# Optimization experiments

Hardware: AMD Instinct MI355X
Metric: run time of the kernel (lower is better)

## Reference

```python
import jax, jax.numpy as jnp
import numpy as np

HIDDEN = 2048
HEADS = 16
HEAD_DIM = HIDDEN // HEADS
BATCH = 2
SEQ = 2048


def setup_inputs() -> dict:
    key = jax.random.key(0)
    ks = jax.random.split(key, 9)
    s = 0.02
    return {
        "x": jax.random.normal(ks[0], (BATCH, SEQ, HIDDEN), dtype=jnp.float32),
        "wq": jax.random.normal(ks[1], (HIDDEN, HIDDEN), dtype=jnp.float32) * s,
        "bq": jax.random.normal(ks[2], (HIDDEN,), dtype=jnp.float32) * s,
        "wk": jax.random.normal(ks[3], (HIDDEN, HIDDEN), dtype=jnp.float32) * s,
        "bk": jax.random.normal(ks[4], (HIDDEN,), dtype=jnp.float32) * s,
        "wv": jax.random.normal(ks[5], (HIDDEN, HIDDEN), dtype=jnp.float32) * s,
        "bv": jax.random.normal(ks[6], (HIDDEN,), dtype=jnp.float32) * s,
        "wo": jax.random.normal(ks[7], (HIDDEN, HIDDEN), dtype=jnp.float32) * s,
        "bo": jax.random.normal(ks[8], (HIDDEN,), dtype=jnp.float32) * s,
    }


def reference(x, wq, bq, wk, bk, wv, bv, wo, bo):
    B, S, _ = x.shape
    scale = jnp.sqrt(jnp.float32(HEAD_DIM))
    # torch Linear: y = x @ W.T + b
    def proj(w, b):
        return (x @ w.T + b).reshape(B, S, HEADS, HEAD_DIM).transpose(0, 2, 1, 3)
    q = proj(wq, bq)  # [B,H,S,D]
    k = proj(wk, bk)
    v = proj(wv, bv)
    scores = jnp.einsum("bhqd,bhkd->bhqk", q, k) / scale  # [B,H,S,S]
    probs = jax.nn.softmax(scores, axis=-1)
    ctx = jnp.einsum("bhqk,bhkd->bhqd", probs, v)  # [B,H,S,D]
    ctx = ctx.transpose(0, 2, 1, 3).reshape(B, S, HIDDEN)
    return ctx @ wo.T + bo
```

## Files before the change

kernel.cpp:

```cpp
#include <hip/hip_runtime.h>

typedef unsigned short u16;
typedef unsigned int   u32;
typedef float  f32x4   __attribute__((ext_vector_type(4)));
typedef __bf16 bf16x8  __attribute__((ext_vector_type(8)));
typedef u16    u16x8   __attribute__((ext_vector_type(8)));
typedef u16    u16x4   __attribute__((ext_vector_type(4)));
typedef u32    u32x2   __attribute__((ext_vector_type(2)));
typedef u32    u32x4   __attribute__((ext_vector_type(4)));

#define HIDDEN 2048
#define SEQ    2048
#define NHEADS 16
#define HD     128
#define BATCH  2
#define QSTR   4096

typedef const __attribute__((address_space(3))) u16* lptr;

__device__ __forceinline__ u16 f2bf(float f) {
  u32 u = __builtin_bit_cast(u32, f);
  u += 0x7FFFu + ((u >> 16) & 1u);
  return (u16)(u >> 16);
}
__device__ __forceinline__ u32 pk2(float a, float b) {
  __bf16 x = (__bf16)a, y = (__bf16)b;
  return (u32)__builtin_bit_cast(u16, x) | ((u32)__builtin_bit_cast(u16, y) << 16);
}
__device__ __forceinline__ bf16x8 ld_frag(const u16* p) {
  return __builtin_bit_cast(bf16x8, *(const u32x4*)p);
}
__device__ __forceinline__ void gload_lds16(const u16* g, u16* l) {
  __builtin_amdgcn_global_load_lds((const __attribute__((address_space(1))) u32*)g,
                                   (__attribute__((address_space(3))) u32*)l, 16, 0, 0);
}

#define DSR(dst, base, lit) \
  asm volatile("ds_read_b128 %0, %1 offset:" lit : "=v"(dst) : "v"(base))

#define MFMA16(d, a, b) d = __builtin_amdgcn_mfma_f32_16x16x32_bf16(a, b, d, 0, 0, 0)

__global__ __launch_bounds__(256) void cvt_kernel(const float* __restrict__ src,
                                                  u16* __restrict__ dst, int n4) {
  int stride = gridDim.x * blockDim.x;
  for (int i = blockIdx.x * blockDim.x + threadIdx.x; i < n4; i += stride) {
    f32x4 v = ((const f32x4*)src)[i];
    u16x4 o;
    o[0] = f2bf(v[0]); o[1] = f2bf(v[1]); o[2] = f2bf(v[2]); o[3] = f2bf(v[3]);
    *(u16x4*)(dst + (size_t)i * 4) = o;
  }
}

__global__ __launch_bounds__(256) void cvt4_kernel(
    const float* __restrict__ s0, const float* __restrict__ s1,
    const float* __restrict__ s2, const float* __restrict__ s3,
    u16* __restrict__ o0, u16* __restrict__ o1,
    u16* __restrict__ o2, u16* __restrict__ o3, int n4) {
  const float* src = (blockIdx.y == 0) ? s0 : (blockIdx.y == 1) ? s1 : (blockIdx.y == 2) ? s2 : s3;
  u16* dst = (blockIdx.y == 0) ? o0 : (blockIdx.y == 1) ? o1 : (blockIdx.y == 2) ? o2 : o3;
  int stride = gridDim.x * blockDim.x;
  for (int i = blockIdx.x * blockDim.x + threadIdx.x; i < n4; i += stride) {
    f32x4 v = ((const f32x4*)src)[i];
    u16x4 o;
    o[0] = f2bf(v[0]); o[1] = f2bf(v[1]); o[2] = f2bf(v[2]); o[3] = f2bf(v[3]);
    *(u16x4*)(dst + (size_t)i * 4) = o;
  }
}

__global__ __launch_bounds__(512, 2) void gemm_qkv(
    const u16* __restrict__ A, const u16* __restrict__ Bt,
    const float* __restrict__ bq, const float* __restrict__ bk,
    const float* __restrict__ bv,
    u16* __restrict__ qk, u16* __restrict__ vtb, float qscale)
{
  __shared__ __attribute__((aligned(16))) u16 As[2][16384];
  __shared__ __attribute__((aligned(16))) u16 Bs[2][12288];

  const int tid  = threadIdx.x;
  const int lane = tid & 63;
  const int wave = tid >> 6;
  const int l15  = lane & 15;
  const int g    = lane >> 4;
  const int wm   = wave >> 2;
  const int wn   = wave & 3;

  const int id  = blockIdx.x;
  const int xcd = id & 7;
  const int c   = id >> 3;
  const int tileN = (xcd * 4 + (c >> 4)) * 192;
  const int tileM = (c & 15) << 8;

  const int srow = tid >> 3;
  const int gch8 = ((tid & 7) ^ (srow & 7)) * 8;
  const u16* agp = A  + (size_t)(tileM + srow) * HIDDEN + gch8;
  const u16* bgp = Bt + (size_t)(tileN + srow) * HIDDEN + gch8;
  u16* asp = (u16*)&As[0][0] + tid * 8;
  u16* bsp = (u16*)&Bs[0][0] + tid * 8;

  auto stage = [&](int buf, int ko) {
    u16* ad = asp + buf * 16384;
    u16* bd = bsp + buf * 12288;
#pragma unroll
    for (int r = 0; r < 4; ++r)
      gload_lds16(agp + (size_t)r * 64 * HIDDEN + ko, ad + r * 4096);
#pragma unroll
    for (int r = 0; r < 3; ++r)
      gload_lds16(bgp + (size_t)r * 64 * HIDDEN + ko, bd + r * 4096);
  };

  const int sw = l15 & 7;
  const int c0 = (g ^ sw) * 8;
  const int c1 = ((g ^ sw) ^ 4) * 8;
  lptr aT = (lptr)&As[0][0] + (size_t)(wm * 128 + l15) * 64;
  lptr bT = (lptr)&Bs[0][0] + (size_t)(wn * 48 + l15) * 64;

  f32x4 acc[8][3] = {};
  bf16x8 Xa[8], Xb[3], Ya[8], Yb[3];

#define ISSUE_SET(Sa, Sb, ab, bb)      \
  DSR(Sa[0], ab, "0");                 \
  DSR(Sa[1], ab, "2048");              \
  DSR(Sa[2], ab, "4096");              \
  DSR(Sa[3], ab, "6144");              \
  DSR(Sa[4], ab, "8192");              \
  DSR(Sa[5], ab, "10240");             \
  DSR(Sa[6], ab, "12288");             \
  DSR(Sa[7], ab, "14336");             \
  DSR(Sb[0], bb, "0");                 \
  DSR(Sb[1], bb, "2048");              \
  DSR(Sb[2], bb, "4096");

#define MFMA24(Sa, Sb)                                                                    \
  _Pragma("unroll")                                                                       \
  for (int mf = 0; mf < 8; ++mf) {                                                        \
    _Pragma("unroll")                                                                     \
    for (int nf = 0; nf < 3; ++nf)                                                        \
      acc[mf][nf] = __builtin_amdgcn_mfma_f32_16x16x32_bf16(Sa[mf], Sb[nf], acc[mf][nf], 0, 0, 0); \
  }

  stage(0, 0);
  stage(1, 64);
  asm volatile("s_waitcnt vmcnt(7)" ::: "memory");
  __builtin_amdgcn_s_barrier();
  __builtin_amdgcn_sched_barrier(0);
  {
    lptr ab = aT + c0;
    lptr bb = bT + c0;
    ISSUE_SET(Xa, Xb, ab, bb)
  }

#pragma unroll 2
  for (int t = 0; t < 32; ++t) {
    const int cur = t & 1;
    lptr aC = aT + cur * 16384;
    lptr bC = bT + cur * 12288;
    {
      lptr ab = aC + c1;
      lptr bb = bC + c1;
      ISSUE_SET(Ya, Yb, ab, bb)
    }
    asm volatile("s_waitcnt lgkmcnt(11)" ::: "memory");
    __builtin_amdgcn_sched_barrier(0);
    __builtin_amdgcn_s_setprio(1);
    MFMA24(Xa, Xb)
    __builtin_amdgcn_s_setprio(0);
    asm volatile("s_waitcnt lgkmcnt(0)" ::: "memory");
    __builtin_amdgcn_sched_barrier(0);
    __builtin_amdgcn_s_setprio(1);
    MFMA24(Ya, Yb)
    __builtin_amdgcn_s_setprio(0);
    __builtin_amdgcn_s_barrier();
    __builtin_amdgcn_sched_barrier(0);
    if (t < 30) {
      stage(cur, (t + 2) * 64);
      asm volatile("s_waitcnt vmcnt(7)" ::: "memory");
    } else {
      asm volatile("s_waitcnt vmcnt(0)" ::: "memory");
    }
    __builtin_amdgcn_s_barrier();
    __builtin_amdgcn_sched_barrier(0);
    if (t < 31) {
      lptr ab = aT + (cur ^ 1) * 16384 + c0;
      lptr bb = bT + (cur ^ 1) * 12288 + c0;
      ISSUE_SET(Xa, Xb, ab, bb)
    }
  }

#pragma unroll
  for (int mi = 0; mi < 8; ++mi) {
#pragma unroll
    for (int ni = 0; ni < 3; ++ni) {
      const int gcb = tileN + wn * 48 + ni * 16;
      const int seg = gcb >> 11;
      const int gc  = gcb + l15;
      const float bvv = ((seg == 0) ? bq : (seg == 1) ? bk : bv)[gc & 2047];
      if (seg < 2) {
        const float scl = (seg == 0) ? qscale : 1.f;
#pragma unroll
        for (int j = 0; j < 4; ++j) {
          const int gr = tileM + wm * 128 + mi * 16 + g * 4 + j;
          qk[(size_t)gr * QSTR + gc] = f2bf((acc[mi][ni][j] + bvv) * scl);
        }
      } else {
        const int dglob = gc - 4096;
        const int hh = dglob >> 7, dd = dglob & 127;
        const int srow0 = tileM + wm * 128 + mi * 16 + g * 4;
        const int bb = srow0 >> 11, ss = srow0 & 2047;
        u16x4 o;
#pragma unroll
        for (int j = 0; j < 4; ++j) o[j] = f2bf(acc[mi][ni][j] + bvv);
        *(u16x4*)(vtb + ((size_t)((bb * NHEADS + hh) * HD + dd)) * SEQ + ss) = o;
      }
    }
  }
#undef ISSUE_SET
#undef MFMA24
}

__global__ __launch_bounds__(256, 2) void gemm_bt(
    const u16* __restrict__ A, const u16* __restrict__ Bt,
    const float* __restrict__ bias, float* __restrict__ Cout,
    int M, int N, int K)
{
  __shared__ __attribute__((aligned(16))) u16 As[128 * 32];
  __shared__ __attribute__((aligned(16))) u16 Bs[128 * 32];
  const int tid  = threadIdx.x;
  const int lane = tid & 63;
  const int wave = tid >> 6;

  const int nbx   = N >> 7;
  const int nby   = M >> 7;
  const int id    = blockIdx.x;
  const int xcd   = id & 7;
  const int c     = id >> 3;
  const int cpx   = nbx >> 3;
  const int tileN = (xcd * cpx + c / nby) << 7;
  const int tileM = (c % nby) << 7;

  const int g = lane >> 4, r = lane & 15;

  const int srow = lane >> 2;
  const int scol = (lane & 3) * 8;
  const u16* ag0 = A  + (size_t)(tileM + wave * 16 + srow) * K + scol;
  const u16* ag1 = ag0 + (size_t)64 * K;
  const u16* bg0 = Bt + (size_t)(tileN + wave * 16 + srow) * K + scol;
  const u16* bg1 = bg0 + (size_t)64 * K;
  u16* as0 = &As[wave * 512];
  u16* as1 = &As[(wave + 4) * 512];
  u16* bs0 = &Bs[wave * 512];
  u16* bs1 = &Bs[(wave + 4) * 512];

  const int wm = wave >> 1, wn = wave & 1;
  const u16* afp = &As[(wm * 64 + r) * 32 + g * 8];
  const u16* bfp = &Bs[(wn * 64 + r) * 32 + g * 8];

  f32x4 acc[4][4] = {};

  for (int kt = 0; kt < K; kt += 32) {
    __syncthreads();
    gload_lds16(ag0 + kt, as0);
    gload_lds16(ag1 + kt, as1);
    gload_lds16(bg0 + kt, bs0);
    gload_lds16(bg1 + kt, bs1);
    __syncthreads();
    bf16x8 af[4], bf[4];
#pragma unroll
    for (int mi = 0; mi < 4; mi++) af[mi] = ld_frag(afp + mi * 512);
#pragma unroll
    for (int ni = 0; ni < 4; ni++) bf[ni] = ld_frag(bfp + ni * 512);
#pragma unroll
    for (int mi = 0; mi < 4; mi++)
#pragma unroll
      for (int ni = 0; ni < 4; ni++)
        acc[mi][ni] = __builtin_amdgcn_mfma_f32_16x16x32_bf16(af[mi], bf[ni], acc[mi][ni], 0, 0, 0);
  }

#pragma unroll
  for (int mi = 0; mi < 4; mi++) {
#pragma unroll
    for (int ni = 0; ni < 4; ni++) {
      const int gc = tileN + wn * 64 + ni * 16 + r;
      const float bv = bias[gc];
#pragma unroll
      for (int j = 0; j < 4; j++) {
        const int gr = tileM + wm * 64 + mi * 16 + g * 4 + j;
        Cout[(size_t)gr * N + gc] = acc[mi][ni][j] + bv;
      }
    }
  }
}

__global__ __launch_bounds__(256, 2) void attn_kernel(
    const u16* __restrict__ QKg, const u16* __restrict__ Vtg, u16* __restrict__ Ctx)
{
  __shared__ __attribute__((aligned(16))) u16 Ks[2][64 * 128];
  __shared__ __attribute__((aligned(16))) u16 Vs[2][128 * 64];

  const int tid  = threadIdx.x;
  const int lane = tid & 63;
  const int wave = tid >> 6;
  const int g4   = lane >> 4;
  const int l15  = lane & 15;

  const int wg = ((blockIdx.x & 7) << 6) + (blockIdx.x >> 3);
  const int bh = wg >> 4;
  const int qt = wg & 15;
  const int b  = bh >> 4, h = bh & 15;

  const u16* Qb  = QKg + (size_t)b * SEQ * QSTR + (size_t)h * HD;
  const u16* Kb  = Qb + 2048;
  const u16* Vth = Vtg + (size_t)bh * HD * SEQ;
  u16* Cb = Ctx + (size_t)b * SEQ * HIDDEN + (size_t)h * HD;

  const int qbase = qt * 128 + wave * 32 + l15;

  bf16x8 qf[2][4];
#pragma unroll
  for (int qs = 0; qs < 2; qs++)
#pragma unroll
    for (int dc = 0; dc < 4; dc++)
      qf[qs][dc] = ld_frag(Qb + (size_t)(qbase + qs * 16) * QSTR + dc * 32 + g4 * 8);

  const int kvp0 = (l15 >> 2) * 8 + (l15 & 3);
  const int msw  = (l15 & 3) | (((l15 >> 2) & 1) << 2);
  const int msw3 = msw & 3;
  const int mk   = (l15 >> 2) & 1;
  const int kcol = (g4 ^ msw3) * 8;

  lptr ksb = (lptr)&Ks[0][0];
  lptr kE0 = ksb + (kvp0      ) * 128 + kcol + mk * 32;
  lptr kO0 = ksb + (kvp0      ) * 128 + kcol + (1 ^ mk) * 32;
  lptr kE1 = ksb + (kvp0 +   4) * 128 + kcol + mk * 32;
  lptr kO1 = ksb + (kvp0 +   4) * 128 + kcol + (1 ^ mk) * 32;
  lptr kE2 = ksb + (kvp0 +  32) * 128 + kcol + mk * 32;
  lptr kO2 = ksb + (kvp0 +  32) * 128 + kcol + (1 ^ mk) * 32;
  lptr kE3 = ksb + (kvp0 +  36) * 128 + kcol + mk * 32;
  lptr kO3 = ksb + (kvp0 +  36) * 128 + kcol + (1 ^ mk) * 32;

  lptr vsb = (lptr)&Vs[0][0];
  lptr vB0 = vsb + l15 * 64 + ((0 * 4 + g4) ^ (l15 & 7)) * 8;
  lptr vB1 = vsb + l15 * 64 + ((1 * 4 + g4) ^ (l15 & 7)) * 8;

  const u16* kg[4];
  const u16* vg[4];
  u16* ksd = (u16*)&Ks[0][0] + tid * 8;
  u16* vsd = (u16*)&Vs[0][0] + tid * 8;
#pragma unroll
  for (int i = 0; i < 4; i++) {
    const int idx = tid + i * 256;
    const int kv = idx >> 4, up = idx & 15;
    const int um = up ^ ((kv & 3) | (((kv >> 3) & 1) << 2));
    kg[i] = Kb + (size_t)kv * QSTR + um * 8;
    const int d = idx >> 3, u = idx & 7;
    const int uv = u ^ (d & 7);
    vg[i] = Vth + (size_t)d * SEQ + uv * 8;
  }

  auto stage = [&](int buf, int kv0) {
    u16* kd = ksd + buf * 8192;
    u16* vd = vsd + buf * 8192;
#pragma unroll
    for (int i = 0; i < 4; i++) gload_lds16(kg[i] + (size_t)kv0 * QSTR, kd + i * 2048);
#pragma unroll
    for (int i = 0; i < 4; i++) gload_lds16(vg[i] + kv0, vd + i * 2048);
  };

  f32x4 ctx[2][8] = {};
  float m_run[2] = {-1e30f, -1e30f};
  float l_run[2] = {0.f, 0.f};

  stage(0, 0);

  const int NT = SEQ / 64;
  for (int t = 0; t < NT; t++) {
    const int buf = t & 1;

    if (t + 1 < NT) {
      stage(buf ^ 1, (t + 1) * 64);
      asm volatile("s_waitcnt vmcnt(8)" ::: "memory");
    } else {
      asm volatile("s_waitcnt vmcnt(0)" ::: "memory");
    }
    __builtin_amdgcn_s_barrier();
    __builtin_amdgcn_sched_barrier(0);

    bf16x8 kf[4][4];
    {
      const int bo = buf * 8192;
      lptr e0 = kE0 + bo, o0 = kO0 + bo, e1 = kE1 + bo, o1 = kO1 + bo;
      lptr e2 = kE2 + bo, o2 = kO2 + bo, e3 = kE3 + bo, o3 = kO3 + bo;
      DSR(kf[0][0], e0, "0"); DSR(kf[0][1], o0, "0"); DSR(kf[0][2], e0, "128"); DSR(kf[0][3], o0, "128");
      DSR(kf[1][0], e1, "0"); DSR(kf[1][1], o1, "0"); DSR(kf[1][2], e1, "128"); DSR(kf[1][3], o1, "128");
      DSR(kf[2][0], e2, "0"); DSR(kf[2][1], o2, "0"); DSR(kf[2][2], e2, "128"); DSR(kf[2][3], o2, "128");
      DSR(kf[3][0], e3, "0"); DSR(kf[3][1], o3, "0"); DSR(kf[3][2], e3, "128"); DSR(kf[3][3], o3, "128");
    }
    f32x4 s[2][4] = {};
    asm volatile("s_waitcnt lgkmcnt(8)" ::: "memory");
    __builtin_amdgcn_sched_barrier(0);
    __builtin_amdgcn_s_setprio(1);
#pragma unroll
    for (int ni = 0; ni < 2; ni++)
#pragma unroll
      for (int dc = 0; dc < 4; dc++) {
        MFMA16(s[0][ni], kf[ni][dc], qf[0][dc]);
        MFMA16(s[1][ni], kf[ni][dc], qf[1][dc]);
      }
    __builtin_amdgcn_sched_barrier(0);
    asm volatile("s_waitcnt lgkmcnt(0)" ::: "memory");
    __builtin_amdgcn_sched_barrier(0);
#pragma unroll
    for (int ni = 2; ni < 4; ni++)
#pragma unroll
      for (int dc = 0; dc < 4; dc++) {
        MFMA16(s[0][ni], kf[ni][dc], qf[0][dc]);
        MFMA16(s[1][ni], kf[ni][dc], qf[1][dc]);
      }
    __builtin_amdgcn_s_setprio(0);
    __builtin_amdgcn_sched_barrier(0);

    float pmax[2];
#pragma unroll
    for (int qs = 0; qs < 2; qs++) {
      float m0 = fmaxf(fmaxf(s[qs][0][0], s[qs][0][1]), fmaxf(s[qs][0][2], s[qs][0][3]));
      float m1 = fmaxf(fmaxf(s[qs][1][0], s[qs][1][1]), fmaxf(s[qs][1][2], s[qs][1][3]));
      float m2 = fmaxf(fmaxf(s[qs][2][0], s[qs][2][1]), fmaxf(s[qs][2][2], s[qs][2][3]));
      float m3 = fmaxf(fmaxf(s[qs][3][0], s[qs][3][1]), fmaxf(s[qs][3][2], s[qs][3][3]));
      pmax[qs] = fmaxf(fmaxf(m0, m1), fmaxf(m2, m3));
      pmax[qs] = fmaxf(pmax[qs], __shfl_xor(pmax[qs], 16));
      pmax[qs] = fmaxf(pmax[qs], __shfl_xor(pmax[qs], 32));
    }
    const bool ok0 = (pmax[0] <= m_run[0] + 8.f);
    const bool ok1 = (pmax[1] <= m_run[1] + 8.f);
    if (!__all(ok0 && ok1)) {
#pragma unroll
      for (int qs = 0; qs < 2; qs++) {
        const float mn = fmaxf(m_run[qs], pmax[qs]);
        const float corr = exp2f(m_run[qs] - mn);
        m_run[qs] = mn;
        l_run[qs] *= corr;
#pragma unroll
        for (int dt = 0; dt < 8; dt++)
#pragma unroll
          for (int j = 0; j < 4; j++) ctx[qs][dt][j] *= corr;
      }
    }
    bf16x8 pfrag[2][2];
#pragma unroll
    for (int qs = 0; qs < 2; qs++) {
      float ps = 0.f;
#pragma unroll
      for (int ni = 0; ni < 4; ni++)
#pragma unroll
        for (int j = 0; j < 4; j++) {
          const float p = exp2f(s[qs][ni][j] - m_run[qs]);
          s[qs][ni][j] = p;
          ps += p;
        }
      ps += __shfl_xor(ps, 16);
      ps += __shfl_xor(ps, 32);
      l_run[qs] += ps;
#pragma unroll
      for (int hh = 0; hh < 2; hh++) {
        u32x4 pw;
        pw[0] = pk2(s[qs][2 * hh][0], s[qs][2 * hh][1]);
        pw[1] = pk2(s[qs][2 * hh][2], s[qs][2 * hh][3]);
        pw[2] = pk2(s[qs][2 * hh + 1][0], s[qs][2 * hh + 1][1]);
        pw[3] = pk2(s[qs][2 * hh + 1][2], s[qs][2 * hh + 1][3]);
        pfrag[qs][hh] = __builtin_bit_cast(bf16x8, pw);
      }
    }
    __builtin_amdgcn_sched_barrier(0);

    bf16x8 vf[2][8];
    {
      lptr v0 = vB0 + buf * 8192;
      lptr v1 = vB1 + buf * 8192;
      DSR(vf[0][0], v0, "0");     DSR(vf[0][1], v0, "2048");
      DSR(vf[0][2], v0, "4096");  DSR(vf[0][3], v0, "6144");
      DSR(vf[0][4], v0, "8192");  DSR(vf[0][5], v0, "10240");
      DSR(vf[0][6], v0, "12288"); DSR(vf[0][7], v0, "14336");
      DSR(vf[1][0], v1, "0");     DSR(vf[1][1], v1, "2048");
      DSR(vf[1][2], v1, "4096");  DSR(vf[1][3], v1, "6144");
      DSR(vf[1][4], v1, "8192");  DSR(vf[1][5], v1, "10240");
      DSR(vf[1][6], v1, "12288"); DSR(vf[1][7], v1, "14336");
    }
    asm volatile("s_waitcnt lgkmcnt(8)" ::: "memory");
    __builtin_amdgcn_sched_barrier(0);
    __builtin_amdgcn_s_setprio(1);
#pragma unroll
    for (int dt = 0; dt < 8; dt++) {
      MFMA16(ctx[0][dt], vf[0][dt], pfrag[0][0]);
      MFMA16(ctx[1][dt], vf[0][dt], pfrag[1][0]);
    }
    __builtin_amdgcn_sched_barrier(0);
    asm volatile("s_waitcnt lgkmcnt(0)" ::: "memory");
    __builtin_amdgcn_sched_barrier(0);
#pragma unroll
    for (int dt = 0; dt < 8; dt++) {
      MFMA16(ctx[0][dt], vf[1][dt], pfrag[0][1]);
      MFMA16(ctx[1][dt], vf[1][dt], pfrag[1][1]);
    }
    __builtin_amdgcn_s_setprio(0);
    __builtin_amdgcn_sched_barrier(0);

    __builtin_amdgcn_s_barrier();
    __builtin_amdgcn_sched_barrier(0);
  }

#pragma unroll
  for (int qs = 0; qs < 2; qs++) {
    const float linv = 1.f / l_run[qs];
    u16* crow = Cb + (size_t)(qbase + qs * 16) * HIDDEN;
#pragma unroll
    for (int dt = 0; dt < 8; dt++) {
      u16x4 o;
#pragma unroll
      for (int j = 0; j < 4; j++) o[j] = f2bf(ctx[qs][dt][j] * linv);
      *(u16x4*)&crow[dt * 16 + g4 * 4] = o;
    }
  }
}

extern "C" void kernel_launch(void* const* d_in, const int* in_sizes, int n_in,
                              void* d_out, int out_size, void* d_ws, size_t ws_size,
                              hipStream_t stream) {
  (void)in_sizes; (void)n_in; (void)out_size; (void)ws_size;
  const float* x  = (const float*)d_in[0];
  const float* wq = (const float*)d_in[1];
  const float* bq = (const float*)d_in[2];
  const float* wk = (const float*)d_in[3];
  const float* bk = (const float*)d_in[4];
  const float* wv = (const float*)d_in[5];
  const float* bv = (const float*)d_in[6];
  const float* wo = (const float*)d_in[7];
  const float* bo = (const float*)d_in[8];

  const size_t NX = (size_t)BATCH * SEQ * HIDDEN;
  const size_t NW = (size_t)HIDDEN * HIDDEN;
  u16* xb   = (u16*)d_ws;
  u16* wqb  = xb  + NX;
  u16* wkb  = wqb + NW;
  u16* wvb  = wkb + NW;
  u16* wob  = wvb + NW;
  u16* qk   = wob + NW;
  u16* vtb  = qk  + 2 * NX;
  u16* ctxb = xb;

  cvt_kernel<<<2048, 256, 0, stream>>>(x, xb, (int)(NX / 4));
  cvt4_kernel<<<dim3(512, 4), 256, 0, stream>>>(wq, wk, wv, wo, wqb, wkb, wvb, wob, (int)(NW / 4));

  const float qscale = 0.12751744174240807f;
  gemm_qkv<<<512, 512, 0, stream>>>(xb, wqb, bq, bk, bv, qk, vtb, qscale);

  attn_kernel<<<512, 256, 0, stream>>>(qk, vtb, ctxb);

  gemm_bt<<<512, 256, 0, stream>>>(ctxb, wob, bo, (float*)d_out, BATCH * SEQ, HIDDEN, HIDDEN);
}
```

Measured before the change: 277.8 us.

## Retile QKV GEMM to 256x128 blocks with BK=32 and defer softmax row-sum reduction

The QKV projection GEMM moves from 256x192 tiles with a 64-wide K step to 256x128 tiles with a 32-wide K step. LDS use per block drops, the launch bound rises to 4 blocks per CU, and the grid grows to 768 blocks, with a new XOR swizzle and a simpler single-buffered fragment load per step. The aim is higher occupancy and better latency hiding, at the cost of lower arithmetic intensity per tile and twice as many barrier-synchronised iterations. Separately, the attention kernel no longer does the cross-lane shuffle reduction of the softmax row sum on every KV tile. It keeps per-lane partial sums and reduces them once at the end, which is valid because all lanes share the same running max.

```diff
diff --git a/kernel.cpp b/kernel.cpp
--- a/kernel.cpp
+++ b/kernel.cpp
@@ -67,130 +67,100 @@
   }
 }
 
-__global__ __launch_bounds__(512, 2) void gemm_qkv(
+__global__ __launch_bounds__(512, 4) void gemm_qkv(
     const u16* __restrict__ A, const u16* __restrict__ Bt,
     const float* __restrict__ bq, const float* __restrict__ bk,
     const float* __restrict__ bv,
     u16* __restrict__ qk, u16* __restrict__ vtb, float qscale)
 {
-  __shared__ __attribute__((aligned(16))) u16 As[2][16384];
-  __shared__ __attribute__((aligned(16))) u16 Bs[2][12288];
+  __shared__ __attribute__((aligned(16))) u16 As[2][8192];
+  __shared__ __attribute__((aligned(16))) u16 Bs[2][4096];
 
   const int tid  = threadIdx.x;
   const int lane = tid & 63;
   const int wave = tid >> 6;
   const int l15  = lane & 15;
   const int g    = lane >> 4;
-  const int wm   = wave >> 2;
-  const int wn   = wave & 3;
+  const int wm   = wave >> 1;
+  const int wn   = wave & 1;
 
   const int id  = blockIdx.x;
   const int xcd = id & 7;
   const int c   = id >> 3;
-  const int tileN = (xcd * 4 + (c >> 4)) * 192;
+  const int tileN = (xcd * 6 + (c >> 4)) << 7;
   const int tileM = (c & 15) << 8;
 
-  const int srow = tid >> 3;
-  const int gch8 = ((tid & 7) ^ (srow & 7)) * 8;
-  const u16* agp = A  + (size_t)(tileM + srow) * HIDDEN + gch8;
-  const u16* bgp = Bt + (size_t)(tileN + srow) * HIDDEN + gch8;
+  const int sr   = tid >> 2;
+  const int su   = tid & 3;
+  const int skey = (sr ^ (sr >> 2)) & 3;
+  const int sgc  = (su ^ skey) * 8;
+  const u16* agp = A  + (size_t)(tileM + sr) * HIDDEN + sgc;
+  const u16* bgp = Bt + (size_t)(tileN + sr) * HIDDEN + sgc;
   u16* asp = (u16*)&As[0][0] + tid * 8;
   u16* bsp = (u16*)&Bs[0][0] + tid * 8;
 
   auto stage = [&](int buf, int ko) {
-    u16* ad = asp + buf * 16384;
-    u16* bd = bsp + buf * 12288;
-#pragma unroll
-    for (int r = 0; r < 4; ++r)
-      gload_lds16(agp + (size_t)r * 64 * HIDDEN + ko, ad + r * 4096);
-#pragma unroll
-    for (int r = 0; r < 3; ++r)
-      gload_lds16(bgp + (size_t)r * 64 * HIDDEN + ko, bd + r * 4096);
+    u16* ad = asp + buf * 8192;
+    gload_lds16(agp + ko, ad);
+    gload_lds16(agp + (size_t)128 * HIDDEN + ko, ad + 4096);
+    gload_lds16(bgp + ko, bsp + buf * 4096);
   };
 
-  const int sw = l15 & 7;
-  const int c0 = (g ^ sw) * 8;
-  const int c1 = ((g ^ sw) ^ 4) * 8;
-  lptr aT = (lptr)&As[0][0] + (size_t)(wm * 128 + l15) * 64;
-  lptr bT = (lptr)&Bs[0][0] + (size_t)(wn * 48 + l15) * 64;
-
-  f32x4 acc[8][3] = {};
-  bf16x8 Xa[8], Xb[3], Ya[8], Yb[3];
-
-#define ISSUE_SET(Sa, Sb, ab, bb)      \
-  DSR(Sa[0], ab, "0");                 \
-  DSR(Sa[1], ab, "2048");              \
-  DSR(Sa[2], ab, "4096");              \
-  DSR(Sa[3], ab, "6144");              \
-  DSR(Sa[4], ab, "8192");              \
-  DSR(Sa[5], ab, "10240");             \
-  DSR(Sa[6], ab, "12288");             \
-  DSR(Sa[7], ab, "14336");             \
-  DSR(Sb[0], bb, "0");                 \
-  DSR(Sb[1], bb, "2048");              \
-  DSR(Sb[2], bb, "4096");
-
-#define MFMA24(Sa, Sb)                                                                    \
-  _Pragma("unroll")                                                                       \
-  for (int mf = 0; mf < 8; ++mf) {                                                        \
-    _Pragma("unroll")                                                                     \
-    for (int nf = 0; nf < 3; ++nf)                                                        \
-      acc[mf][nf] = __builtin_amdgcn_mfma_f32_16x16x32_bf16(Sa[mf], Sb[nf], acc[mf][nf], 0, 0, 0); \
-  }
+  const int fkey = (l15 ^ (l15 >> 2)) & 3;
+  const int kch  = (g ^ fkey) * 8;
+  lptr aT = (lptr)&As[0][0] + (size_t)(wm * 64 + l15) * 32 + kch;
+  lptr bT = (lptr)&Bs[0][0] + (size_t)(wn * 64 + l15) * 32 + kch;
+
+  f32x4 acc[4][4] = {};
+  bf16x8 af[4], bf[4];
+
+#define ISSUE8(ab, bb)                                                              \
+  DSR(af[0], ab, "0"); DSR(af[1], ab, "1024"); DSR(af[2], ab, "2048"); DSR(af[3], ab, "3072"); \
+  DSR(bf[0], bb, "0"); DSR(bf[1], bb, "1024"); DSR(bf[2], bb, "2048"); DSR(bf[3], bb, "3072");
 
   stage(0, 0);
-  stage(1, 64);
-  asm volatile("s_waitcnt vmcnt(7)" ::: "memory");
+  stage(1, 32);
+  asm volatile("s_waitcnt vmcnt(3)" ::: "memory");
   __builtin_amdgcn_s_barrier();
   __builtin_amdgcn_sched_barrier(0);
-  {
-    lptr ab = aT + c0;
-    lptr bb = bT + c0;
-    ISSUE_SET(Xa, Xb, ab, bb)
-  }
+  { lptr ab = aT, bb = bT; ISSUE8(ab, bb) }
 
 #pragma unroll 2
-  for (int t = 0; t < 32; ++t) {
+  for (int t = 0; t < 64; ++t) {
     const int cur = t & 1;
-    lptr aC = aT + cur * 16384;
-    lptr bC = bT + cur * 12288;
-    {
-      lptr ab = aC + c1;
-      lptr bb = bC + c1;
-      ISSUE_SET(Ya, Yb, ab, bb)
-    }
-    asm volatile("s_waitcnt lgkmcnt(11)" ::: "memory");
-    __builtin_amdgcn_sched_barrier(0);
+    asm volatile("s_waitcnt lgkmcnt(0)" ::: "memory");
+    __builtin_amdgcn_sched_barrier(0);
+    __builtin_amdgcn_s_barrier();
+    __builtin_amdgcn_sched_barrier(0);
+    if (t < 62) stage(cur, (t + 2) * 32);
     __builtin_amdgcn_s_setprio(1);
-    MFMA24(Xa, Xb)
+#pragma unroll
+    for (int mf = 0; mf < 4; ++mf)
+#pragma unroll
+      for (int nf = 0; nf < 4; ++nf)
+        MFMA16(acc[mf][nf], af[mf], bf[nf]);
     __builtin_amdgcn_s_setprio(0);
-    asm volatile("s_waitcnt lgkmcnt(0)" ::: "memory");
-    __builtin_amdgcn_sched_barrier(0);
-    __builtin_amdgcn_s_setprio(1);
-    MFMA24(Ya, Yb)
-    __builtin_amdgcn_s_setprio(0);
-    __builtin_amdgcn_s_barrier();
-    __builtin_amdgcn_sched_barrier(0);
-    if (t < 30) {
-      stage(cur, (t + 2) * 64);
-      asm volatile("s_waitcnt vmcnt(7)" ::: "memory");
+    __builtin_amdgcn_sched_barrier(0);
+    if (t < 62) {
+      asm volatile("s_waitcnt vmcnt(3)" ::: "memory");
     } else {
       asm volatile("s_waitcnt vmcnt(0)" ::: "memory");
     }
     __builtin_amdgcn_s_barrier();
     __builtin_amdgcn_sched_barrier(0);
-    if (t < 31) {
-      lptr ab = aT + (cur ^ 1) * 16384 + c0;
-      lptr bb = bT + (cur ^ 1) * 12288 + c0;
-      ISSUE_SET(Xa, Xb, ab, bb)
-    }
-  }
-
-#pragma unroll
-  for (int mi = 0; mi < 8; ++mi) {
-#pragma unroll
-    for (int ni = 0; ni < 3; ++ni) {
-      const int gcb = tileN + wn * 48 + ni * 16;
+    if (t < 63) {
+      lptr ab = aT + (cur ^ 1) * 8192;
+      lptr bb = bT + (cur ^ 1) * 4096;
+      ISSUE8(ab, bb)
+    }
+  }
+#undef ISSUE8
+
+#pragma unroll
+  for (int mf = 0; mf < 4; ++mf) {
+#pragma unroll
+    for (int nf = 0; nf < 4; ++nf) {
+      const int gcb = tileN + wn * 64 + nf * 16;
       const int seg = gcb >> 11;
       const int gc  = gcb + l15;
       const float bvv = ((seg == 0) ? bq : (seg == 1) ? bk : bv)[gc & 2047];
@@ -198,23 +168,21 @@
         const float scl = (seg == 0) ? qscale : 1.f;
 #pragma unroll
         for (int j = 0; j < 4; ++j) {
-          const int gr = tileM + wm * 128 + mi * 16 + g * 4 + j;
-          qk[(size_t)gr * QSTR + gc] = f2bf((acc[mi][ni][j] + bvv) * scl);
+          const int gr = tileM + wm * 64 + mf * 16 + g * 4 + j;
+          qk[(size_t)gr * QSTR + gc] = f2bf((acc[mf][nf][j] + bvv) * scl);
         }
       } else {
         const int dglob = gc - 4096;
         const int hh = dglob >> 7, dd = dglob & 127;
-        const int srow0 = tileM + wm * 128 + mi * 16 + g * 4;
+        const int srow0 = tileM + wm * 64 + mf * 16 + g * 4;
         const int bb = srow0 >> 11, ss = srow0 & 2047;
         u16x4 o;
 #pragma unroll
-        for (int j = 0; j < 4; ++j) o[j] = f2bf(acc[mi][ni][j] + bvv);
+        for (int j = 0; j < 4; ++j) o[j] = f2bf(acc[mf][nf][j] + bvv);
         *(u16x4*)(vtb + ((size_t)((bb * NHEADS + hh) * HD + dd)) * SEQ + ss) = o;
       }
     }
   }
-#undef ISSUE_SET
-#undef MFMA24
 }
 
 __global__ __launch_bounds__(256, 2) void gemm_bt(
@@ -456,8 +424,6 @@
           s[qs][ni][j] = p;
           ps += p;
         }
-      ps += __shfl_xor(ps, 16);
-      ps += __shfl_xor(ps, 32);
       l_run[qs] += ps;
 #pragma unroll
       for (int hh = 0; hh < 2; hh++) {
@@ -509,7 +475,10 @@
 
 #pragma unroll
   for (int qs = 0; qs < 2; qs++) {
-    const float linv = 1.f / l_run[qs];
+    float lt = l_run[qs];
+    lt += __shfl_xor(lt, 16);
+    lt += __shfl_xor(lt, 32);
+    const float linv = 1.f / lt;
     u16* crow = Cb + (size_t)(qbase + qs * 16) * HIDDEN;
 #pragma unroll
     for (int dt = 0; dt < 8; dt++) {
@@ -550,7 +519,7 @@
   cvt4_kernel<<<dim3(512, 4), 256, 0, stream>>>(wq, wk, wv, wo, wqb, wkb, wvb, wob, (int)(NW / 4));
 
   const float qscale = 0.12751744174240807f;
-  gemm_qkv<<<512, 512, 0, stream>>>(xb, wqb, bq, bk, bv, qk, vtb, qscale);
+  gemm_qkv<<<768, 512, 0, stream>>>(xb, wqb, bq, bk, bv, qk, vtb, qscale);
 
   attn_kernel<<<512, 256, 0, stream>>>(qk, vtb, ctxb);
 
```

New measurement: 284.3 us. +2.3%, slower.
